# Optimization experiments

Measured on AMD Instinct MI355X. Metric: run time of the kernel, lower is better.

## Reference

```python
import jax, jax.numpy as jnp
import numpy as np

B_, L_, H_, N_ = 8, 1024, 1024, 64

def setup_inputs() -> dict:
    key = jax.random.key(0)
    k1, k2, k3, k4 = jax.random.split(key, 4)
    return {
        "samples": jax.random.normal(k1, (B_, L_, 3 * H_), dtype=jnp.float32),
        "label_one_hot": jax.random.uniform(k2, (B_, L_, N_), dtype=jnp.float32),
        "predict": jax.random.normal(k3, (B_, L_, N_), dtype=jnp.float32),
        "W": jax.random.normal(k4, (H_, 3 * H_), dtype=jnp.float32) * (1.0 / np.sqrt(3 * H_)),
        "b_proj": jnp.zeros((H_,), dtype=jnp.float32),
    }

def reference(samples, label_one_hot, predict, W, b_proj):
    # projection: Linear(3H -> H)
    s = jnp.einsum("blk,hk->blh", samples, W) + b_proj          # [b,L,H]
    # dense similarity graph with diagonal masked out, row-softmax
    graph = jnp.einsum("blh,bmh->blm", s, s)                     # [b,L,L]
    L = graph.shape[1]
    eye = jnp.eye(L, dtype=graph.dtype)
    A = jax.nn.softmax(graph - 1e5 * eye, axis=-1)               # [b,L,L]
    # centered masked labels
    sup = label_one_hot
    row_has = (jnp.sum(sup, axis=-1) > 0.5).astype(sup.dtype)    # [b,L]
    total = jnp.sum(row_has, axis=-1)[:, None]                   # [b,1]
    avg = (jnp.sum(sup, axis=-2) / total)[:, None, :]            # [b,1,N]
    B0 = (sup - avg) * row_has[..., None]                        # [b,L,N]
    # diagonal inverse-degree scaling (elementwise, no dense diag matmul)
    d = 1.0 / (jnp.sum(A, axis=-1) + 1e-10)                      # [b,L]
    P = d[:, :, None] * jnp.swapaxes(A, -1, -2)                  # [b,L,L]
    Db = d[:, :, None] * B0                                      # [b,L,N]
    # 6-step power-iteration scan with residual injection at t==3
    ut = jnp.zeros_like(B0)
    for t in range(1, 7):
        ut = jnp.einsum("blm,bmn->bln", P, ut) + Db
        if t == 3:
            ut = ut + predict  # dropout is identity in eval mode
    return ut

if __name__ == "__main__":
    out = reference(**setup_inputs())
    print(out.shape, out.dtype)
```

## Files before the change

kernel.cpp:

```cpp
#include <hip/hip_runtime.h>


typedef _Float16 f16_t;
typedef f16_t f16x4 __attribute__((ext_vector_type(4)));
typedef f16_t f16x8 __attribute__((ext_vector_type(8)));
typedef float floatx4 __attribute__((ext_vector_type(4)));

__device__ __forceinline__ void async_copy16(const void* g, void* l) {
  __builtin_amdgcn_global_load_lds(
      (const __attribute__((address_space(1))) void*)g,
      (__attribute__((address_space(3))) void*)l, 16, 0, 0);
}

__device__ __forceinline__ f16_t hi_of(float x) { return (f16_t)x; }
__device__ __forceinline__ f16_t lo_of(float x, f16_t h) {
  return (f16_t)(x - (float)h);
}

__global__ __launch_bounds__(256) void prep_kernel(
    const float* __restrict__ W, f16_t* __restrict__ Whi, f16_t* __restrict__ Wlo,
    const float* __restrict__ samples, f16_t* __restrict__ SampH)
{
  const int bx = blockIdx.x, tid = threadIdx.x;
  if (bx < 3072) {
    const int i = bx * 256 + tid;
    float4 v = ((const float4*)W)[i];
    v.x *= 32.f; v.y *= 32.f; v.z *= 32.f; v.w *= 32.f;
    f16x4 h, l;
    f16_t h0 = hi_of(v.x); h[0] = h0; l[0] = lo_of(v.x, h0);
    f16_t h1 = hi_of(v.y); h[1] = h1; l[1] = lo_of(v.y, h1);
    f16_t h2 = hi_of(v.z); h[2] = h2; l[2] = lo_of(v.z, h2);
    f16_t h3 = hi_of(v.w); h[3] = h3; l[3] = lo_of(v.w, h3);
    *(f16x4*)(Whi + (size_t)i * 4) = h;
    *(f16x4*)(Wlo + (size_t)i * 4) = l;
  } else {
    const int i = (bx - 3072) * 256 + tid;
    const float4 v = ((const float4*)samples)[i];
    f16x4 h;
    h[0] = (f16_t)v.x; h[1] = (f16_t)v.y; h[2] = (f16_t)v.z; h[3] = (f16_t)v.w;
    *(f16x4*)(SampH + (size_t)i * 4) = h;
  }
}

struct Frags {
  f16x8 a[8];
  f16x8 bh0, bh1, bl0, bl1;
};

#define DSR(dst_, addr_, OFFSTR_) \
  asm volatile("ds_read_b128 %0, %1 offset:" OFFSTR_ : "=v"(dst_) : "v"(addr_))

__device__ __forceinline__ void read_frags_asm(unsigned sa, unsigned sb,
                                               Frags& f) {
  DSR(f.bh0, sb, "0");
  DSR(f.bh1, sb, "1024");
  DSR(f.bl0, sb, "8192");
  DSR(f.bl1, sb, "9216");
  DSR(f.a[0], sa, "0");
  DSR(f.a[1], sa, "1024");
  DSR(f.a[2], sa, "2048");
  DSR(f.a[3], sa, "3072");
  DSR(f.a[4], sa, "4096");
  DSR(f.a[5], sa, "5120");
  DSR(f.a[6], sa, "6144");
  DSR(f.a[7], sa, "7168");
}

__global__ __launch_bounds__(512, 2) void gemm1_pipe(
    const f16_t* __restrict__ Ag,
    const f16_t* __restrict__ BhG, const f16_t* __restrict__ BlG,
    const float* __restrict__ bias,
    f16_t* __restrict__ Chi, f16_t* __restrict__ Clo,
    int N, int K, float cscale)
{
  __shared__ __align__(16) char smem[131072];

  const int tid = threadIdx.x;
  const int lane = tid & 63;
  const int wave = tid >> 6;
  const int wm = wave >> 2;
  const int wn = wave & 3;
  const int bid0 = blockIdx.y * 8 + blockIdx.x;
  const int xk = bid0 & 7, xj = bid0 >> 3;
  const int m0 = ((xk >> 1) * 8 + (xj >> 2)) * 256;
  const int n0 = ((xk & 1) * 4 + (xj & 3)) * 128;
  const int fr = lane & 15;
  const int lch = lane >> 4;

  const int gA0 = tid;
  const int gA1 = tid + 512;
  const int rA0 = gA0 >> 2, lcA0 = (gA0 & 3) ^ ((rA0 >> 1) & 3);
  const int rA1 = gA1 >> 2, lcA1 = (gA1 & 3) ^ ((rA1 >> 1) & 3);
  const int rB = tid >> 2, lcB = (tid & 3) ^ ((rB >> 1) & 3);
  const f16_t* aSrc0 = Ag + (size_t)(m0 + rA0) * K + lcA0 * 8;
  const f16_t* aSrc1 = Ag + (size_t)(m0 + rA1) * K + lcA1 * 8;
  const f16_t* bhSrc = BhG + (size_t)(n0 + rB) * K + lcB * 8;
  const f16_t* blSrc = BlG + (size_t)(n0 + rB) * K + lcB * 8;
  char* ldsA0 = smem + gA0 * 16;
  char* ldsA1 = smem + gA1 * 16;
  char* ldsBh = smem + 16384 + (size_t)tid * 16;
  char* ldsBl = smem + 24576 + (size_t)tid * 16;

  const int swz = (lch ^ ((fr >> 1) & 3)) * 16;
  const int aoff = (wm * 128 + fr) * 64 + swz;
  const int boff = (wn * 32 + fr) * 64 + swz;
  const unsigned ldsBase =
      (unsigned)(size_t)(__attribute__((address_space(3))) char*)smem;
  const unsigned aA0 = ldsBase + (unsigned)aoff;
  const unsigned aA1 = aA0 + 32768u;
  const unsigned aA2 = aA0 + 65536u;
  const unsigned aA3 = aA0 + 98304u;
  const unsigned bA0 = ldsBase + 16384u + (unsigned)boff;
  const unsigned bA1 = bA0 + 32768u;
  const unsigned bA2 = bA0 + 65536u;
  const unsigned bA3 = bA0 + 98304u;

  floatx4 acc[8][2] = {};
  const int NS = K >> 5;

#define STAGE(SS_, SLOT_)                                     \
  do {                                                        \
    int ss = (SS_); if (ss >= NS) ss -= NS;                   \
    const int k0 = ss * 32;                                   \
    async_copy16(aSrc0 + k0, ldsA0 + (SLOT_) * 32768);        \
    async_copy16(aSrc1 + k0, ldsA1 + (SLOT_) * 32768);        \
    async_copy16(bhSrc + k0, ldsBh + (SLOT_) * 32768);        \
    async_copy16(blSrc + k0, ldsBl + (SLOT_) * 32768);        \
  } while (0)

#define MFMA8(F_, P_)                                                                                               \
  do {                                                                                                              \
    acc[2*(P_)][0]   = __builtin_amdgcn_mfma_f32_16x16x32_f16((F_).a[2*(P_)],   (F_).bh0, acc[2*(P_)][0],   0,0,0); \
    acc[2*(P_)][1]   = __builtin_amdgcn_mfma_f32_16x16x32_f16((F_).a[2*(P_)],   (F_).bh1, acc[2*(P_)][1],   0,0,0); \
    acc[2*(P_)+1][0] = __builtin_amdgcn_mfma_f32_16x16x32_f16((F_).a[2*(P_)+1], (F_).bh0, acc[2*(P_)+1][0], 0,0,0); \
    acc[2*(P_)+1][1] = __builtin_amdgcn_mfma_f32_16x16x32_f16((F_).a[2*(P_)+1], (F_).bh1, acc[2*(P_)+1][1], 0,0,0); \
    acc[2*(P_)][0]   = __builtin_amdgcn_mfma_f32_16x16x32_f16((F_).a[2*(P_)],   (F_).bl0, acc[2*(P_)][0],   0,0,0); \
    acc[2*(P_)][1]   = __builtin_amdgcn_mfma_f32_16x16x32_f16((F_).a[2*(P_)],   (F_).bl1, acc[2*(P_)][1],   0,0,0); \
    acc[2*(P_)+1][0] = __builtin_amdgcn_mfma_f32_16x16x32_f16((F_).a[2*(P_)+1], (F_).bl0, acc[2*(P_)+1][0], 0,0,0); \
    acc[2*(P_)+1][1] = __builtin_amdgcn_mfma_f32_16x16x32_f16((F_).a[2*(P_)+1], (F_).bl1, acc[2*(P_)+1][1], 0,0,0); \
  } while (0)

#define SB0 __builtin_amdgcn_sched_barrier(0)

#define HALF(SPRE_, SLOTPRE_, ARD_, BRD_, FRD_, FMM_)            \
  do {                                                           \
    STAGE(SPRE_, SLOTPRE_);                                      \
    asm volatile("s_waitcnt vmcnt(8)" ::: "memory");             \
    __builtin_amdgcn_s_barrier();                                \
    DSR(FRD_.bh0, BRD_, "0");                                    \
    DSR(FRD_.bh1, BRD_, "1024");                                 \
    DSR(FRD_.bl0, BRD_, "8192");                                 \
    SB0;                                                         \
    asm volatile("s_waitcnt lgkmcnt(3)" ::: "memory");           \
    SB0;                                                         \
    __builtin_amdgcn_s_setprio(1);                               \
    MFMA8(FMM_, 0);                                              \
    __builtin_amdgcn_s_setprio(0);                               \
    SB0;                                                         \
    DSR(FRD_.bl1, BRD_, "9216");                                 \
    DSR(FRD_.a[0], ARD_, "0");                                   \
    DSR(FRD_.a[1], ARD_, "1024");                                \
    SB0;                                                         \
    __builtin_amdgcn_s_setprio(1);                               \
    MFMA8(FMM_, 1);                                              \
    __builtin_amdgcn_s_setprio(0);                               \
    SB0;                                                         \
    DSR(FRD_.a[2], ARD_, "2048");                                \
    DSR(FRD_.a[3], ARD_, "3072");                                \
    DSR(FRD_.a[4], ARD_, "4096");                                \
    SB0;                                                         \
    __builtin_amdgcn_s_setprio(1);                               \
    MFMA8(FMM_, 2);                                              \
    __builtin_amdgcn_s_setprio(0);                               \
    SB0;                                                         \
    DSR(FRD_.a[5], ARD_, "5120");                                \
    DSR(FRD_.a[6], ARD_, "6144");                                \
    DSR(FRD_.a[7], ARD_, "7168");                                \
    SB0;                                                         \
    __builtin_amdgcn_s_setprio(1);                               \
    MFMA8(FMM_, 3);                                              \
    __builtin_amdgcn_s_setprio(0);                               \
    SB0;                                                         \
  } while (0)

  Frags f0, f1;

  STAGE(0, 0); STAGE(1, 1); STAGE(2, 2);
  asm volatile("s_waitcnt vmcnt(8)" ::: "memory");
  __builtin_amdgcn_s_barrier();
  read_frags_asm(aA0, bA0, f0);
  SB0;

  for (int s = 0; s < NS; s += 4) {
    HALF(s + 3, 3, aA1, bA1, f1, f0);
    HALF(s + 4, 0, aA2, bA2, f0, f1);
    HALF(s + 5, 1, aA3, bA3, f1, f0);
    HALF(s + 6, 2, aA0, bA0, f0, f1);
  }
  asm volatile("s_waitcnt vmcnt(0)" ::: "memory");
#undef HALF
#undef STAGE
#undef MFMA8

  const int mr = (lane >> 4) * 4;
#pragma unroll
  for (int j = 0; j < 2; ++j) {
    const int n = n0 + wn * 32 + j * 16 + fr;
    const float bj = bias[n];
#pragma unroll
    for (int i = 0; i < 8; ++i) {
#pragma unroll
      for (int r = 0; r < 4; ++r) {
        const int m = m0 + wm * 128 + i * 16 + mr + r;
        float v = acc[i][j][r] * cscale + bj;
        f16_t h = hi_of(v);
        Chi[(size_t)m * N + n] = h;
        Clo[(size_t)m * N + n] = lo_of(v, h);
      }
    }
  }
}

struct Frags2 {
  f16x8 a[4];
  f16x8 bh[4];
  f16x8 bl[4];
};

__global__ __launch_bounds__(256, 2) void gemm2_pipe(
    const f16_t* __restrict__ Sh, const f16_t* __restrict__ Sl,
    float* __restrict__ Gf)
{
  const int K = 1024, N = 1024;
  const int batch = blockIdx.x & 7;
  const long long bo = (long long)batch * (1024LL * 1024);
  const f16_t* Ahi = Sh + bo;
  const f16_t* Bhi = Sh + bo;
  const f16_t* Blo = Sl + bo;
  float* Cf = Gf + bo;

  __shared__ __align__(16) char smem[73728];

  const int tid = threadIdx.x;
  const int lane = tid & 63;
  const int wave = tid >> 6;
  const int wm = wave >> 1, wn = wave & 1;

  int idx = blockIdx.x >> 3, ti = 0, accu = 0;
  while (accu + ti + 1 <= idx) { accu += ti + 1; ++ti; }
  const int m0 = ti * 128;
  const int n0 = (idx - accu) * 128;

  const int fr = lane & 15;
  const int lch = lane >> 4;

  const int gA0 = tid, gA1 = tid + 256;
  const int rA0 = gA0 >> 2, cA0 = (gA0 & 3) ^ ((rA0 >> 1) & 3);
  const int rA1 = gA1 >> 2, cA1 = (gA1 & 3) ^ ((rA1 >> 1) & 3);
  const f16_t* aSr0 = Ahi + (size_t)(m0 + rA0) * K + cA0 * 8;
  const f16_t* aSr1 = Ahi + (size_t)(m0 + rA1) * K + cA1 * 8;
  const f16_t* hSr0 = Bhi + (size_t)(n0 + rA0) * K + cA0 * 8;
  const f16_t* hSr1 = Bhi + (size_t)(n0 + rA1) * K + cA1 * 8;
  const f16_t* lSr0 = Blo + (size_t)(n0 + rA0) * K + cA0 * 8;
  const f16_t* lSr1 = Blo + (size_t)(n0 + rA1) * K + cA1 * 8;
  char* dA0 = smem + gA0 * 16;
  char* dA1 = smem + gA1 * 16;
  char* dH0 = smem + 8192 + gA0 * 16;
  char* dH1 = smem + 8192 + gA1 * 16;
  char* dL0 = smem + 16384 + gA0 * 16;
  char* dL1 = smem + 16384 + gA1 * 16;

  const int swz16 = (lch ^ ((fr >> 1) & 3)) * 16;
  const int aoff = (wm * 64 + fr) * 64 + swz16;
  const int boff = (wn * 64 + fr) * 64 + swz16;
  const unsigned ldsBase =
      (unsigned)(size_t)(__attribute__((address_space(3))) char*)smem;
  const unsigned aT0 = ldsBase + (unsigned)aoff;
  const unsigned aT1 = aT0 + 24576u;
  const unsigned aT2 = aT0 + 49152u;
  const unsigned bT0 = ldsBase + 8192u + (unsigned)boff;
  const unsigned bT1 = bT0 + 24576u;
  const unsigned bT2 = bT0 + 49152u;

  floatx4 acc[4][4] = {};
  const int NS = 32;

#define STAGE2(SS_, SLOT_)                                    \
  do {                                                        \
    int ss = (SS_); if (ss >= NS) ss -= NS;                   \
    const int k0 = ss * 32;                                   \
    async_copy16(aSr0 + k0, dA0 + (SLOT_) * 24576);           \
    async_copy16(aSr1 + k0, dA1 + (SLOT_) * 24576);           \
    async_copy16(hSr0 + k0, dH0 + (SLOT_) * 24576);           \
    async_copy16(hSr1 + k0, dH1 + (SLOT_) * 24576);           \
    async_copy16(lSr0 + k0, dL0 + (SLOT_) * 24576);           \
    async_copy16(lSr1 + k0, dL1 + (SLOT_) * 24576);           \
  } while (0)

#define MFMA8_2(F_, P_)                                                                              \
  do {                                                                                               \
    acc[0][P_] = __builtin_amdgcn_mfma_f32_16x16x32_f16((F_).a[0], (F_).bh[P_], acc[0][P_], 0,0,0);  \
    acc[1][P_] = __builtin_amdgcn_mfma_f32_16x16x32_f16((F_).a[1], (F_).bh[P_], acc[1][P_], 0,0,0);  \
    acc[2][P_] = __builtin_amdgcn_mfma_f32_16x16x32_f16((F_).a[2], (F_).bh[P_], acc[2][P_], 0,0,0);  \
    acc[3][P_] = __builtin_amdgcn_mfma_f32_16x16x32_f16((F_).a[3], (F_).bh[P_], acc[3][P_], 0,0,0);  \
    acc[0][P_] = __builtin_amdgcn_mfma_f32_16x16x32_f16((F_).a[0], (F_).bl[P_], acc[0][P_], 0,0,0);  \
    acc[1][P_] = __builtin_amdgcn_mfma_f32_16x16x32_f16((F_).a[1], (F_).bl[P_], acc[1][P_], 0,0,0);  \
    acc[2][P_] = __builtin_amdgcn_mfma_f32_16x16x32_f16((F_).a[2], (F_).bl[P_], acc[2][P_], 0,0,0);  \
    acc[3][P_] = __builtin_amdgcn_mfma_f32_16x16x32_f16((F_).a[3], (F_).bl[P_], acc[3][P_], 0,0,0);  \
  } while (0)

#define SB0 __builtin_amdgcn_sched_barrier(0)

#define GR3(SPRE_, SLOTPRE_, ARD_, BRD_, FRD_, FMM_)             \
  do {                                                           \
    STAGE2(SPRE_, SLOTPRE_);                                     \
    asm volatile("s_waitcnt vmcnt(6)" ::: "memory");             \
    __builtin_amdgcn_s_barrier();                                \
    DSR(FRD_.bh[0], BRD_, "0");                                  \
    DSR(FRD_.bh[1], BRD_, "1024");                               \
    DSR(FRD_.bh[2], BRD_, "2048");                               \
    SB0;                                                         \
    asm volatile("s_waitcnt lgkmcnt(3)" ::: "memory");           \
    SB0;                                                         \
    __builtin_amdgcn_s_setprio(1);                               \
    MFMA8_2(FMM_, 0);                                            \
    __builtin_amdgcn_s_setprio(0);                               \
    SB0;                                                         \
    DSR(FRD_.bh[3], BRD_, "3072");                               \
    DSR(FRD_.bl[0], BRD_, "8192");                               \
    DSR(FRD_.bl[1], BRD_, "9216");                               \
    SB0;                                                         \
    __builtin_amdgcn_s_setprio(1);                               \
    MFMA8_2(FMM_, 1);                                            \
    __builtin_amdgcn_s_setprio(0);                               \
    SB0;                                                         \
    DSR(FRD_.bl[2], BRD_, "10240");                              \
    DSR(FRD_.bl[3], BRD_, "11264");                              \
    DSR(FRD_.a[0], ARD_, "0");                                   \
    SB0;                                                         \
    __builtin_amdgcn_s_setprio(1);                               \
    MFMA8_2(FMM_, 2);                                            \
    __builtin_amdgcn_s_setprio(0);                               \
    SB0;                                                         \
    DSR(FRD_.a[1], ARD_, "1024");                                \
    DSR(FRD_.a[2], ARD_, "2048");                                \
    DSR(FRD_.a[3], ARD_, "3072");                                \
    SB0;                                                         \
    __builtin_amdgcn_s_setprio(1);                               \
    MFMA8_2(FMM_, 3);                                            \
    __builtin_amdgcn_s_setprio(0);                               \
    SB0;                                                         \
  } while (0)

  Frags2 f0, f1;

  STAGE2(0, 0); STAGE2(1, 1);
  asm volatile("s_waitcnt vmcnt(6)" ::: "memory");
  __builtin_amdgcn_s_barrier();
  DSR(f0.bh[0], bT0, "0");
  DSR(f0.bh[1], bT0, "1024");
  DSR(f0.bh[2], bT0, "2048");
  DSR(f0.bh[3], bT0, "3072");
  DSR(f0.bl[0], bT0, "8192");
  DSR(f0.bl[1], bT0, "9216");
  DSR(f0.bl[2], bT0, "10240");
  DSR(f0.bl[3], bT0, "11264");
  DSR(f0.a[0], aT0, "0");
  DSR(f0.a[1], aT0, "1024");
  DSR(f0.a[2], aT0, "2048");
  DSR(f0.a[3], aT0, "3072");
  SB0;

  for (int s = 0; s < 30; s += 6) {
    GR3(s + 2, 2, aT1, bT1, f1, f0);
    GR3(s + 3, 0, aT2, bT2, f0, f1);
    GR3(s + 4, 1, aT0, bT0, f1, f0);
    GR3(s + 5, 2, aT1, bT1, f0, f1);
    GR3(s + 6, 0, aT2, bT2, f1, f0);
    GR3(s + 7, 1, aT0, bT0, f0, f1);
  }
  asm volatile("s_waitcnt vmcnt(0)" ::: "memory");
  __builtin_amdgcn_s_barrier();
  DSR(f1.bh[0], bT1, "0");
  DSR(f1.bh[1], bT1, "1024");
  DSR(f1.bh[2], bT1, "2048");
  DSR(f1.bh[3], bT1, "3072");
  DSR(f1.bl[0], bT1, "8192");
  DSR(f1.bl[1], bT1, "9216");
  DSR(f1.bl[2], bT1, "10240");
  DSR(f1.bl[3], bT1, "11264");
  DSR(f1.a[0], aT1, "0");
  DSR(f1.a[1], aT1, "1024");
  DSR(f1.a[2], aT1, "2048");
  DSR(f1.a[3], aT1, "3072");
  SB0;
  asm volatile("s_waitcnt lgkmcnt(12)" ::: "memory");
  SB0;
  __builtin_amdgcn_s_setprio(1);
  MFMA8_2(f0, 0); MFMA8_2(f0, 1); MFMA8_2(f0, 2); MFMA8_2(f0, 3);
  __builtin_amdgcn_s_setprio(0);
  SB0;
  asm volatile("s_waitcnt lgkmcnt(0)" ::: "memory");
  SB0;
  __builtin_amdgcn_s_setprio(1);
  MFMA8_2(f1, 0); MFMA8_2(f1, 1); MFMA8_2(f1, 2); MFMA8_2(f1, 3);
  __builtin_amdgcn_s_setprio(0);
#undef GR3
#undef MFMA8_2
#undef STAGE2

  const int mr = (lane >> 4) * 4;
#pragma unroll
  for (int j = 0; j < 4; ++j) {
    const int n = n0 + wn * 64 + j * 16 + fr;
#pragma unroll
    for (int i = 0; i < 4; ++i) {
#pragma unroll
      for (int r = 0; r < 4; ++r) {
        const int m = m0 + wm * 64 + i * 16 + mr + r;
        float v = acc[i][j][r];
        if (m == n) v -= 1e5f;
        Cf[(size_t)m * N + n] = v;
      }
    }
  }

  if (m0 != n0) {
    float* T = (float*)smem;
#pragma unroll
    for (int mc = 0; mc < 4; ++mc) {
      __syncthreads();
      if (wm == (mc >> 1)) {
        const int ibase = (mc & 1) * 2;
#pragma unroll
        for (int di = 0; di < 2; ++di) {
#pragma unroll
          for (int j = 0; j < 4; ++j) {
            const int nl = wn * 64 + j * 16 + fr;
#pragma unroll
            for (int r = 0; r < 4; ++r) {
              const int mloc = di * 16 + mr + r;
              T[nl * 36 + mloc] = acc[ibase + di][j][r];
            }
          }
        }
      }
      __syncthreads();
      const int row = tid >> 1, half = tid & 1;
      const float* src = &T[row * 36 + half * 16];
      float* dst = Cf + (size_t)(n0 + row) * N + m0 + mc * 32 + half * 16;
#pragma unroll
      for (int q = 0; q < 16; ++q) dst[q] = src[q];
    }
  }
}

__global__ __launch_bounds__(256) void rowstats_kernel(
    const float* __restrict__ G, float* __restrict__ mx, float* __restrict__ inv)
{
  __shared__ float redm[4][4], reds[4][4], mxsh[4];
  const int tid = threadIdx.x;
  const int r0 = blockIdx.x * 4;
  const float* g = G + (size_t)r0 * 1024;
  const float4 v0 = ((const float4*)g)[tid];
  const float4 v1 = ((const float4*)(g + 1024))[tid];
  const float4 v2 = ((const float4*)(g + 2048))[tid];
  const float4 v3 = ((const float4*)(g + 3072))[tid];

  float m0 = fmaxf(fmaxf(v0.x, v0.y), fmaxf(v0.z, v0.w));
  float m1 = fmaxf(fmaxf(v1.x, v1.y), fmaxf(v1.z, v1.w));
  float m2 = fmaxf(fmaxf(v2.x, v2.y), fmaxf(v2.z, v2.w));
  float m3 = fmaxf(fmaxf(v3.x, v3.y), fmaxf(v3.z, v3.w));
#pragma unroll
  for (int off = 32; off > 0; off >>= 1) {
    m0 = fmaxf(m0, __shfl_down(m0, off));
    m1 = fmaxf(m1, __shfl_down(m1, off));
    m2 = fmaxf(m2, __shfl_down(m2, off));
    m3 = fmaxf(m3, __shfl_down(m3, off));
  }
  if ((tid & 63) == 0) {
    redm[0][tid >> 6] = m0; redm[1][tid >> 6] = m1;
    redm[2][tid >> 6] = m2; redm[3][tid >> 6] = m3;
  }
  __syncthreads();
  if (tid < 4)
    mxsh[tid] = fmaxf(fmaxf(redm[tid][0], redm[tid][1]),
                      fmaxf(redm[tid][2], redm[tid][3]));
  __syncthreads();
  const float M0 = mxsh[0], M1 = mxsh[1], M2 = mxsh[2], M3 = mxsh[3];

  float s0 = __expf(v0.x - M0) + __expf(v0.y - M0) + __expf(v0.z - M0) + __expf(v0.w - M0);
  float s1 = __expf(v1.x - M1) + __expf(v1.y - M1) + __expf(v1.z - M1) + __expf(v1.w - M1);
  float s2 = __expf(v2.x - M2) + __expf(v2.y - M2) + __expf(v2.z - M2) + __expf(v2.w - M2);
  float s3 = __expf(v3.x - M3) + __expf(v3.y - M3) + __expf(v3.z - M3) + __expf(v3.w - M3);
#pragma unroll
  for (int off = 32; off > 0; off >>= 1) {
    s0 += __shfl_down(s0, off);
    s1 += __shfl_down(s1, off);
    s2 += __shfl_down(s2, off);
    s3 += __shfl_down(s3, off);
  }
  if ((tid & 63) == 0) {
    reds[0][tid >> 6] = s0; reds[1][tid >> 6] = s1;
    reds[2][tid >> 6] = s2; reds[3][tid >> 6] = s3;
  }
  __syncthreads();
  if (tid < 4) {
    mx[r0 + tid] = mxsh[tid];
    inv[r0 + tid] = 1.0f /
        (reds[tid][0] + reds[tid][1] + reds[tid][2] + reds[tid][3]);
  }
}

__global__ __launch_bounds__(256) void make_at_kernel(
    const float* __restrict__ G, const float* __restrict__ mx,
    const float* __restrict__ inv, f16_t* __restrict__ At)
{
  const int r0 = blockIdx.x * 4;
  const int b = r0 >> 10;
  const int tid = threadIdx.x;
  const float4 m = ((const float4*)(mx + b * 1024))[tid];
  const float4 iv = ((const float4*)(inv + b * 1024))[tid];
#pragma unroll
  for (int k = 0; k < 4; ++k) {
    const float4 g = ((const float4*)(G + (size_t)(r0 + k) * 1024))[tid];
    f16x4 o;
    o[0] = (f16_t)(__expf(g.x - m.x) * iv.x);
    o[1] = (f16_t)(__expf(g.y - m.y) * iv.y);
    o[2] = (f16_t)(__expf(g.z - m.z) * iv.z);
    o[3] = (f16_t)(__expf(g.w - m.w) * iv.w);
    *(f16x4*)(At + (size_t)(r0 + k) * 1024 + tid * 4) = o;
  }
}

__global__ __launch_bounds__(256) void db_stats(
    const float* __restrict__ sup, float* __restrict__ colpart,
    float* __restrict__ totalpart)
{
  const int b = blockIdx.x >> 4, chunk = blockIdx.x & 15;
  const int tid = threadIdx.x;
  const int r = tid >> 2, q = tid & 3;
  const float* s = sup + ((size_t)b * 1024 + chunk * 64 + r) * 64 + q * 16;
  const float4 x0 = ((const float4*)s)[0];
  const float4 x1 = ((const float4*)s)[1];
  const float4 x2 = ((const float4*)s)[2];
  const float4 x3 = ((const float4*)s)[3];

  float rs = (x0.x + x0.y + x0.z + x0.w) + (x1.x + x1.y + x1.z + x1.w) +
             (x2.x + x2.y + x2.z + x2.w) + (x3.x + x3.y + x3.z + x3.w);
  rs += __shfl_xor(rs, 1);
  rs += __shfl_xor(rs, 2);
  const float rh = (rs > 0.5f) ? 1.f : 0.f;

  __shared__ float colp[64];
  __shared__ float tp[4];
  if (tid < 64) colp[tid] = 0.f;
  __syncthreads();
  atomicAdd(&colp[q * 16 + 0], x0.x);  atomicAdd(&colp[q * 16 + 1], x0.y);
  atomicAdd(&colp[q * 16 + 2], x0.z);  atomicAdd(&colp[q * 16 + 3], x0.w);
  atomicAdd(&colp[q * 16 + 4], x1.x);  atomicAdd(&colp[q * 16 + 5], x1.y);
  atomicAdd(&colp[q * 16 + 6], x1.z);  atomicAdd(&colp[q * 16 + 7], x1.w);
  atomicAdd(&colp[q * 16 + 8], x2.x);  atomicAdd(&colp[q * 16 + 9], x2.y);
  atomicAdd(&colp[q * 16 + 10], x2.z); atomicAdd(&colp[q * 16 + 11], x2.w);
  atomicAdd(&colp[q * 16 + 12], x3.x); atomicAdd(&colp[q * 16 + 13], x3.y);
  atomicAdd(&colp[q * 16 + 14], x3.z); atomicAdd(&colp[q * 16 + 15], x3.w);

  float ts = (q == 0) ? rh : 0.f;
#pragma unroll
  for (int off = 32; off > 0; off >>= 1) ts += __shfl_down(ts, off);
  if ((tid & 63) == 0) tp[tid >> 6] = ts;
  __syncthreads();
  if (tid < 64) colpart[((size_t)b * 16 + chunk) * 64 + tid] = colp[tid];
  if (tid == 0) totalpart[b * 16 + chunk] = tp[0] + tp[1] + tp[2] + tp[3];
}

__global__ __launch_bounds__(256) void db_apply(
    const float* __restrict__ sup, const float* __restrict__ colpart,
    const float* __restrict__ totalpart,
    float* __restrict__ Db, f16_t* __restrict__ DbT)
{
  const int b = blockIdx.x >> 4, chunk = blockIdx.x & 15;
  const int tid = threadIdx.x;
  const int r = tid >> 2, q = tid & 3;

  __shared__ float avgsh[64];
  __shared__ float totsh;
  __shared__ f16_t DbTs[64 * 72];

  float a = 0.f;
  if (tid < 64) {
#pragma unroll
    for (int c = 0; c < 16; ++c) a += colpart[((size_t)b * 16 + c) * 64 + tid];
  }
  if (tid == 0) {
    float tt = 0.f;
#pragma unroll
    for (int c = 0; c < 16; ++c) tt += totalpart[b * 16 + c];
    totsh = tt;
  }
  __syncthreads();
  if (tid < 64) avgsh[tid] = a / totsh;
  __syncthreads();

  const size_t rowoff = ((size_t)b * 1024 + chunk * 64 + r) * 64 + q * 16;
  const float* s = sup + rowoff;
  float4 x0 = ((const float4*)s)[0];
  float4 x1 = ((const float4*)s)[1];
  float4 x2 = ((const float4*)s)[2];
  float4 x3 = ((const float4*)s)[3];

  float rs = (x0.x + x0.y + x0.z + x0.w) + (x1.x + x1.y + x1.z + x1.w) +
             (x2.x + x2.y + x2.z + x2.w) + (x3.x + x3.y + x3.z + x3.w);
  rs += __shfl_xor(rs, 1);
  rs += __shfl_xor(rs, 2);
  const float rh = (rs > 0.5f) ? 1.f : 0.f;

  const int nb = q * 16;
  x0.x = (x0.x - avgsh[nb + 0]) * rh;  x0.y = (x0.y - avgsh[nb + 1]) * rh;
  x0.z = (x0.z - avgsh[nb + 2]) * rh;  x0.w = (x0.w - avgsh[nb + 3]) * rh;
  x1.x = (x1.x - avgsh[nb + 4]) * rh;  x1.y = (x1.y - avgsh[nb + 5]) * rh;
  x1.z = (x1.z - avgsh[nb + 6]) * rh;  x1.w = (x1.w - avgsh[nb + 7]) * rh;
  x2.x = (x2.x - avgsh[nb + 8]) * rh;  x2.y = (x2.y - avgsh[nb + 9]) * rh;
  x2.z = (x2.z - avgsh[nb + 10]) * rh; x2.w = (x2.w - avgsh[nb + 11]) * rh;
  x3.x = (x3.x - avgsh[nb + 12]) * rh; x3.y = (x3.y - avgsh[nb + 13]) * rh;
  x3.z = (x3.z - avgsh[nb + 14]) * rh; x3.w = (x3.w - avgsh[nb + 15]) * rh;

  float* d = Db + rowoff;
  ((float4*)d)[0] = x0; ((float4*)d)[1] = x1;
  ((float4*)d)[2] = x2; ((float4*)d)[3] = x3;

  DbTs[(nb + 0) * 72 + r] = (f16_t)x0.x;  DbTs[(nb + 1) * 72 + r] = (f16_t)x0.y;
  DbTs[(nb + 2) * 72 + r] = (f16_t)x0.z;  DbTs[(nb + 3) * 72 + r] = (f16_t)x0.w;
  DbTs[(nb + 4) * 72 + r] = (f16_t)x1.x;  DbTs[(nb + 5) * 72 + r] = (f16_t)x1.y;
  DbTs[(nb + 6) * 72 + r] = (f16_t)x1.z;  DbTs[(nb + 7) * 72 + r] = (f16_t)x1.w;
  DbTs[(nb + 8) * 72 + r] = (f16_t)x2.x;  DbTs[(nb + 9) * 72 + r] = (f16_t)x2.y;
  DbTs[(nb + 10) * 72 + r] = (f16_t)x2.z; DbTs[(nb + 11) * 72 + r] = (f16_t)x2.w;
  DbTs[(nb + 12) * 72 + r] = (f16_t)x3.x; DbTs[(nb + 13) * 72 + r] = (f16_t)x3.y;
  DbTs[(nb + 14) * 72 + r] = (f16_t)x3.z; DbTs[(nb + 15) * 72 + r] = (f16_t)x3.w;
  __syncthreads();

  const int n = tid >> 2, seg = tid & 3;
  const f16_t* src = &DbTs[n * 72 + seg * 16];
  f16_t* dst = DbT + ((size_t)b * 64 + n) * 1024 + chunk * 64 + seg * 16;
  *(f16x8*)dst = *(const f16x8*)src;
  *(f16x8*)(dst + 8) = *(const f16x8*)(src + 8);
}

template <int PRED, int FINAL>
__global__ __launch_bounds__(256) void iter_step(
    const f16_t* __restrict__ At, const f16_t* __restrict__ UT,
    const float* __restrict__ Db, const float* __restrict__ Pred,
    f16_t* __restrict__ UTn, float* __restrict__ OutF)
{
  const int L = 1024, Nn = 64;
  const int b = blockIdx.x & 7, l0 = (blockIdx.x >> 3) * 32;
  At += (size_t)b * L * L;
  UT += (size_t)b * Nn * L;

  __shared__ __align__(16) char smem[131072];

  const int tid = threadIdx.x;
  const int lane = tid & 63;
  const int wave = tid >> 6;
  const int fr = lane & 15;
  const int lch = lane >> 4;
  const int mwb = wave * 256;

  int g_, rw_, sc_;
  g_ = lane;        rw_ = g_ >> 3; sc_ = (g_ & 7) ^ (rw_ & 7);
  const f16_t* aS0 = At + (size_t)(l0 + rw_) * L + mwb + sc_ * 8;
  g_ = lane + 64;   rw_ = g_ >> 3; sc_ = (g_ & 7) ^ (rw_ & 7);
  const f16_t* aS1 = At + (size_t)(l0 + rw_) * L + mwb + sc_ * 8;
  g_ = lane + 128;  rw_ = g_ >> 3; sc_ = (g_ & 7) ^ (rw_ & 7);
  const f16_t* aS2 = At + (size_t)(l0 + rw_) * L + mwb + sc_ * 8;
  g_ = lane + 192;  rw_ = g_ >> 3; sc_ = (g_ & 7) ^ (rw_ & 7);
  const f16_t* aS3 = At + (size_t)(l0 + rw_) * L + mwb + sc_ * 8;
  g_ = lane;        rw_ = g_ >> 3; sc_ = (g_ & 7) ^ (rw_ & 7);
  const f16_t* uS0 = UT + (size_t)rw_ * L + mwb + sc_ * 8;
  g_ = lane + 64;   rw_ = g_ >> 3; sc_ = (g_ & 7) ^ (rw_ & 7);
  const f16_t* uS1 = UT + (size_t)rw_ * L + mwb + sc_ * 8;
  g_ = lane + 128;  rw_ = g_ >> 3; sc_ = (g_ & 7) ^ (rw_ & 7);
  const f16_t* uS2 = UT + (size_t)rw_ * L + mwb + sc_ * 8;
  g_ = lane + 192;  rw_ = g_ >> 3; sc_ = (g_ & 7) ^ (rw_ & 7);
  const f16_t* uS3 = UT + (size_t)rw_ * L + mwb + sc_ * 8;
  g_ = lane + 256;  rw_ = g_ >> 3; sc_ = (g_ & 7) ^ (rw_ & 7);
  const f16_t* uS4 = UT + (size_t)rw_ * L + mwb + sc_ * 8;
  g_ = lane + 320;  rw_ = g_ >> 3; sc_ = (g_ & 7) ^ (rw_ & 7);
  const f16_t* uS5 = UT + (size_t)rw_ * L + mwb + sc_ * 8;
  g_ = lane + 384;  rw_ = g_ >> 3; sc_ = (g_ & 7) ^ (rw_ & 7);
  const f16_t* uS6 = UT + (size_t)rw_ * L + mwb + sc_ * 8;
  g_ = lane + 448;  rw_ = g_ >> 3; sc_ = (g_ & 7) ^ (rw_ & 7);
  const f16_t* uS7 = UT + (size_t)rw_ * L + mwb + sc_ * 8;

  char* stA = smem + wave * 24576;
  char* stU = stA + 4096;

  const int offK0 = fr * 128 + ((lch ^ (fr & 7)) * 16);
  const int offK1 = fr * 128 + (((4 + lch) ^ (fr & 7)) * 16);

  floatx4 acc[2][4] = {};

#define STG(M0_, BUF_)                                        \
  do {                                                        \
    char* dA = stA + (BUF_) * 12288;                          \
    char* dU = stU + (BUF_) * 12288;                          \
    async_copy16(aS0 + (M0_), dA + lane * 16);                \
    async_copy16(aS1 + (M0_), dA + 1024 + lane * 16);         \
    async_copy16(aS2 + (M0_), dA + 2048 + lane * 16);         \
    async_copy16(aS3 + (M0_), dA + 3072 + lane * 16);         \
    async_copy16(uS0 + (M0_), dU + lane * 16);                \
    async_copy16(uS1 + (M0_), dU + 1024 + lane * 16);         \
    async_copy16(uS2 + (M0_), dU + 2048 + lane * 16);         \
    async_copy16(uS3 + (M0_), dU + 3072 + lane * 16);         \
    async_copy16(uS4 + (M0_), dU + 4096 + lane * 16);         \
    async_copy16(uS5 + (M0_), dU + 5120 + lane * 16);         \
    async_copy16(uS6 + (M0_), dU + 6144 + lane * 16);         \
    async_copy16(uS7 + (M0_), dU + 7168 + lane * 16);         \
  } while (0)

#define LD8(b_, o_) (*(const f16x8*)((b_) + (o_)))
#define MM(A_, U_, C_) C_ = __builtin_amdgcn_mfma_f32_16x16x32_f16(A_, U_, C_, 0, 0, 0)

#define CHUNK(BUF_)                                                       \
  do {                                                                    \
    const char* cA = stA + (BUF_) * 12288;                                \
    const char* cU = stU + (BUF_) * 12288;                                \
    f16x8 a00 = LD8(cA, offK0), a01 = LD8(cA, offK1);                     \
    f16x8 a10 = LD8(cA, offK0 + 2048), a11 = LD8(cA, offK1 + 2048);       \
    f16x8 u00 = LD8(cU, offK0), u01 = LD8(cU, offK1);                     \
    f16x8 u10 = LD8(cU, offK0 + 2048), u11 = LD8(cU, offK1 + 2048);       \
    f16x8 u20 = LD8(cU, offK0 + 4096), u21 = LD8(cU, offK1 + 4096);       \
    f16x8 u30 = LD8(cU, offK0 + 6144), u31 = LD8(cU, offK1 + 6144);       \
    MM(a00, u00, acc[0][0]); MM(a00, u10, acc[0][1]);                     \
    MM(a00, u20, acc[0][2]); MM(a00, u30, acc[0][3]);                     \
    MM(a10, u00, acc[1][0]); MM(a10, u10, acc[1][1]);                     \
    MM(a10, u20, acc[1][2]); MM(a10, u30, acc[1][3]);                     \
    MM(a01, u01, acc[0][0]); MM(a01, u11, acc[0][1]);                     \
    MM(a01, u21, acc[0][2]); MM(a01, u31, acc[0][3]);                     \
    MM(a11, u01, acc[1][0]); MM(a11, u11, acc[1][1]);                     \
    MM(a11, u21, acc[1][2]); MM(a11, u31, acc[1][3]);                     \
  } while (0)

#define SB0 __builtin_amdgcn_sched_barrier(0)

  STG(0, 0);
  STG(64, 1);
  asm volatile("s_waitcnt vmcnt(12)" ::: "memory");
  SB0;
  CHUNK(0);
  SB0;
  STG(128, 0);
  asm volatile("s_waitcnt vmcnt(12)" ::: "memory");
  SB0;
  CHUNK(1);
  SB0;
  STG(192, 1);
  asm volatile("s_waitcnt vmcnt(12)" ::: "memory");
  SB0;
  CHUNK(0);
  SB0;
  asm volatile("s_waitcnt vmcnt(0)" ::: "memory");
  SB0;
  CHUNK(1);
#undef CHUNK
#undef STG

  float* P = (float*)(smem + 98304) + wave * 2048;
  const int mr = (lane >> 4) * 4;
#pragma unroll
  for (int li = 0; li < 2; ++li)
#pragma unroll
    for (int j = 0; j < 4; ++j)
#pragma unroll
      for (int r = 0; r < 4; ++r)
        P[(li * 16 + mr + r) * 64 + j * 16 + fr] = acc[li][j][r];
  __syncthreads();

  const float* P0 = (const float*)(smem + 98304);
  const size_t obase = ((size_t)b * L + l0) * Nn;
  f16_t* OutS = (f16_t*)smem;
#pragma unroll
  for (int it = 0; it < 2; ++it) {
    const int e4 = it * 256 + tid;
    const int l = e4 >> 4, n4 = (e4 & 15) * 4;
    const int eo = l * 64 + n4;
    float4 v = *(const float4*)(P0 + eo);
    const float4 p1 = *(const float4*)(P0 + 2048 + eo);
    const float4 p2 = *(const float4*)(P0 + 4096 + eo);
    const float4 p3 = *(const float4*)(P0 + 6144 + eo);
    v.x += p1.x; v.y += p1.y; v.z += p1.z; v.w += p1.w;
    v.x += p2.x; v.y += p2.y; v.z += p2.z; v.w += p2.w;
    v.x += p3.x; v.y += p3.y; v.z += p3.z; v.w += p3.w;
    const float4 d = *(const float4*)(Db + obase + eo);
    v.x += d.x; v.y += d.y; v.z += d.z; v.w += d.w;
    if (PRED) {
      const float4 p = *(const float4*)(Pred + obase + eo);
      v.x += p.x; v.y += p.y; v.z += p.z; v.w += p.w;
    }
    if (FINAL) {
      *(float4*)(OutF + obase + eo) = v;
    } else {
      OutS[(n4 + 0) * 40 + l] = (f16_t)v.x;
      OutS[(n4 + 1) * 40 + l] = (f16_t)v.y;
      OutS[(n4 + 2) * 40 + l] = (f16_t)v.z;
      OutS[(n4 + 3) * 40 + l] = (f16_t)v.w;
    }
  }
  if (!FINAL) {
    __syncthreads();
    f16_t* dst = UTn + (size_t)b * Nn * L + l0;
    const int n = tid >> 2, lc = (tid & 3) * 8;
    *(f16x8*)(dst + (size_t)n * L + lc) = *(const f16x8*)&OutS[n * 40 + lc];
  }
#undef SB0
#undef LD8
#undef MM
}

extern "C" void kernel_launch(void* const* d_in, const int* in_sizes, int n_in,
                              void* d_out, int out_size, void* d_ws, size_t ws_size,
                              hipStream_t stream) {
  const float* samples = (const float*)d_in[0];
  const float* label   = (const float*)d_in[1];
  const float* predict = (const float*)d_in[2];
  const float* W       = (const float*)d_in[3];
  const float* bproj   = (const float*)d_in[4];
  float* out = (float*)d_out;

  char* ws = (char*)d_ws;
  f16_t* Whi = (f16_t*)ws;
  f16_t* Wlo = (f16_t*)(ws + 6291456);
  float* mx  = (float*)ws;
  float* inv = (float*)(ws + 32768);
  float* Db  = (float*)(ws + 65536);
  f16_t* DbT = (f16_t*)(ws + 65536 + 2097152);
  f16_t* UTa = (f16_t*)(ws + 65536 + 3145728);
  f16_t* UTb = (f16_t*)(ws + 65536 + 4194304);
  float* colpart   = (float*)(ws + 5308416);
  float* totalpart = (float*)(ws + 5308416 + 32768);
  f16_t* SampH = (f16_t*)(ws + 12582912);
  float* G     = (float*)(ws + 12582912);
  f16_t* Shi = (f16_t*)(ws + 62914560);
  f16_t* Slo = (f16_t*)(ws + 62914560 + 16777216);
  f16_t* At  = Shi;

  prep_kernel<<<dim3(27648), 256, 0, stream>>>(W, Whi, Wlo, samples, SampH);

  gemm1_pipe<<<dim3(8, 32), 512, 0, stream>>>(
      SampH, Whi, Wlo, bproj, Shi, Slo, 1024, 3072, 1.0f / 32.0f);

  gemm2_pipe<<<dim3(288), 256, 0, stream>>>(Shi, Slo, G);

  rowstats_kernel<<<2048, 256, 0, stream>>>(G, mx, inv);
  make_at_kernel<<<2048, 256, 0, stream>>>(G, mx, inv, At);

  db_stats<<<128, 256, 0, stream>>>(label, colpart, totalpart);
  db_apply<<<128, 256, 0, stream>>>(label, colpart, totalpart, Db, DbT);

  iter_step<0, 0><<<dim3(256), 256, 0, stream>>>(At, DbT, Db, nullptr, UTa, nullptr);
  iter_step<1, 0><<<dim3(256), 256, 0, stream>>>(At, UTa, Db, predict, UTb, nullptr);
  iter_step<0, 0><<<dim3(256), 256, 0, stream>>>(At, UTb, Db, nullptr, UTa, nullptr);
  iter_step<0, 0><<<dim3(256), 256, 0, stream>>>(At, UTa, Db, nullptr, UTb, nullptr);
  iter_step<0, 1><<<dim3(256), 256, 0, stream>>>(At, UTb, Db, nullptr, nullptr, out);
}
```

Before: 339.2 us.

## Load B fragments directly from global into registers, bypassing LDS

The projection GEMM now stages only the A tile through LDS. Each wave loads its B (W hi/lo) fragments straight from global memory into registers with global_load_dwordx4, issued one stage ahead. This halves LDS usage to 64KB and removes the LDS writes and reads for B. In exchange, B reuse across the waves sharing the same wn is lost, so global/L2 traffic goes up, and the vmcnt accounting becomes more fragile.

```diff
diff --git a/kernel.cpp b/kernel.cpp
--- a/kernel.cpp
+++ b/kernel.cpp
@@ -50,21 +50,8 @@
 #define DSR(dst_, addr_, OFFSTR_) \
   asm volatile("ds_read_b128 %0, %1 offset:" OFFSTR_ : "=v"(dst_) : "v"(addr_))
 
-__device__ __forceinline__ void read_frags_asm(unsigned sa, unsigned sb,
-                                               Frags& f) {
-  DSR(f.bh0, sb, "0");
-  DSR(f.bh1, sb, "1024");
-  DSR(f.bl0, sb, "8192");
-  DSR(f.bl1, sb, "9216");
-  DSR(f.a[0], sa, "0");
-  DSR(f.a[1], sa, "1024");
-  DSR(f.a[2], sa, "2048");
-  DSR(f.a[3], sa, "3072");
-  DSR(f.a[4], sa, "4096");
-  DSR(f.a[5], sa, "5120");
-  DSR(f.a[6], sa, "6144");
-  DSR(f.a[7], sa, "7168");
-}
+#define GLD(dst_, ptr_) \
+  asm volatile("global_load_dwordx4 %0, %1, off" : "=v"(dst_) : "v"(ptr_))
 
 __global__ __launch_bounds__(512, 2) void gemm1_pipe(
     const f16_t* __restrict__ Ag,
@@ -73,7 +60,7 @@
     f16_t* __restrict__ Chi, f16_t* __restrict__ Clo,
     int N, int K, float cscale)
 {
-  __shared__ __align__(16) char smem[131072];
+  __shared__ __align__(16) char smem[65536];
 
   const int tid = threadIdx.x;
   const int lane = tid & 63;
@@ -91,41 +78,44 @@
   const int gA1 = tid + 512;
   const int rA0 = gA0 >> 2, lcA0 = (gA0 & 3) ^ ((rA0 >> 1) & 3);
   const int rA1 = gA1 >> 2, lcA1 = (gA1 & 3) ^ ((rA1 >> 1) & 3);
-  const int rB = tid >> 2, lcB = (tid & 3) ^ ((rB >> 1) & 3);
   const f16_t* aSrc0 = Ag + (size_t)(m0 + rA0) * K + lcA0 * 8;
   const f16_t* aSrc1 = Ag + (size_t)(m0 + rA1) * K + lcA1 * 8;
-  const f16_t* bhSrc = BhG + (size_t)(n0 + rB) * K + lcB * 8;
-  const f16_t* blSrc = BlG + (size_t)(n0 + rB) * K + lcB * 8;
   char* ldsA0 = smem + gA0 * 16;
   char* ldsA1 = smem + gA1 * 16;
-  char* ldsBh = smem + 16384 + (size_t)tid * 16;
-  char* ldsBl = smem + 24576 + (size_t)tid * 16;
+
+  const f16_t* bh0Src = BhG + (size_t)(n0 + wn * 32 + fr) * K + lch * 8;
+  const f16_t* bh1Src = BhG + (size_t)(n0 + wn * 32 + 16 + fr) * K + lch * 8;
+  const f16_t* bl0Src = BlG + (size_t)(n0 + wn * 32 + fr) * K + lch * 8;
+  const f16_t* bl1Src = BlG + (size_t)(n0 + wn * 32 + 16 + fr) * K + lch * 8;
 
   const int swz = (lch ^ ((fr >> 1) & 3)) * 16;
   const int aoff = (wm * 128 + fr) * 64 + swz;
-  const int boff = (wn * 32 + fr) * 64 + swz;
   const unsigned ldsBase =
       (unsigned)(size_t)(__attribute__((address_space(3))) char*)smem;
   const unsigned aA0 = ldsBase + (unsigned)aoff;
-  const unsigned aA1 = aA0 + 32768u;
-  const unsigned aA2 = aA0 + 65536u;
-  const unsigned aA3 = aA0 + 98304u;
-  const unsigned bA0 = ldsBase + 16384u + (unsigned)boff;
-  const unsigned bA1 = bA0 + 32768u;
-  const unsigned bA2 = bA0 + 65536u;
-  const unsigned bA3 = bA0 + 98304u;
+  const unsigned aA1 = aA0 + 16384u;
+  const unsigned aA2 = aA0 + 32768u;
+  const unsigned aA3 = aA0 + 49152u;
 
   floatx4 acc[8][2] = {};
   const int NS = K >> 5;
 
-#define STAGE(SS_, SLOT_)                                     \
+#define STAGEA(SS_, SLOT_)                                    \
   do {                                                        \
     int ss = (SS_); if (ss >= NS) ss -= NS;                   \
     const int k0 = ss * 32;                                   \
-    async_copy16(aSrc0 + k0, ldsA0 + (SLOT_) * 32768);        \
-    async_copy16(aSrc1 + k0, ldsA1 + (SLOT_) * 32768);        \
-    async_copy16(bhSrc + k0, ldsBh + (SLOT_) * 32768);        \
-    async_copy16(blSrc + k0, ldsBl + (SLOT_) * 32768);        \
+    async_copy16(aSrc0 + k0, ldsA0 + (SLOT_) * 16384);        \
+    async_copy16(aSrc1 + k0, ldsA1 + (SLOT_) * 16384);        \
+  } while (0)
+
+#define LOADB(SS_, FRD_)                                      \
+  do {                                                        \
+    int sb = (SS_); if (sb >= NS) sb -= NS;                   \
+    const int kb = sb * 32;                                   \
+    GLD(FRD_.bh0, bh0Src + kb);                               \
+    GLD(FRD_.bh1, bh1Src + kb);                               \
+    GLD(FRD_.bl0, bl0Src + kb);                               \
+    GLD(FRD_.bl1, bl1Src + kb);                               \
   } while (0)
 
 #define MFMA8(F_, P_)                                                                                               \
@@ -142,38 +132,35 @@
 
 #define SB0 __builtin_amdgcn_sched_barrier(0)
 
-#define HALF(SPRE_, SLOTPRE_, ARD_, BRD_, FRD_, FMM_)            \
+#define HALF(SPRE_, SLOTPRE_, ARD_, FRD_, FMM_)                  \
   do {                                                           \
-    STAGE(SPRE_, SLOTPRE_);                                      \
-    asm volatile("s_waitcnt vmcnt(8)" ::: "memory");             \
+    LOADB((SPRE_) - 2, FRD_);                                    \
+    STAGEA(SPRE_, SLOTPRE_);                                     \
+    asm volatile("s_waitcnt vmcnt(12)" ::: "memory");            \
     __builtin_amdgcn_s_barrier();                                \
-    DSR(FRD_.bh0, BRD_, "0");                                    \
-    DSR(FRD_.bh1, BRD_, "1024");                                 \
-    DSR(FRD_.bl0, BRD_, "8192");                                 \
-    SB0;                                                         \
-    asm volatile("s_waitcnt lgkmcnt(3)" ::: "memory");           \
+    DSR(FRD_.a[0], ARD_, "0");                                   \
+    DSR(FRD_.a[1], ARD_, "1024");                                \
+    SB0;                                                         \
+    asm volatile("s_waitcnt lgkmcnt(2) vmcnt(8)" ::: "memory");  \
     SB0;                                                         \
     __builtin_amdgcn_s_setprio(1);                               \
     MFMA8(FMM_, 0);                                              \
     __builtin_amdgcn_s_setprio(0);                               \
     SB0;                                                         \
-    DSR(FRD_.bl1, BRD_, "9216");                                 \
-    DSR(FRD_.a[0], ARD_, "0");                                   \
-    DSR(FRD_.a[1], ARD_, "1024");                                \
+    DSR(FRD_.a[2], ARD_, "2048");                                \
+    DSR(FRD_.a[3], ARD_, "3072");                                \
     SB0;                                                         \
     __builtin_amdgcn_s_setprio(1);                               \
     MFMA8(FMM_, 1);                                              \
     __builtin_amdgcn_s_setprio(0);                               \
     SB0;                                                         \
-    DSR(FRD_.a[2], ARD_, "2048");                                \
-    DSR(FRD_.a[3], ARD_, "3072");                                \
     DSR(FRD_.a[4], ARD_, "4096");                                \
+    DSR(FRD_.a[5], ARD_, "5120");                                \
     SB0;                                                         \
     __builtin_amdgcn_s_setprio(1);                               \
     MFMA8(FMM_, 2);                                              \
     __builtin_amdgcn_s_setprio(0);                               \
     SB0;                                                         \
-    DSR(FRD_.a[5], ARD_, "5120");                                \
     DSR(FRD_.a[6], ARD_, "6144");                                \
     DSR(FRD_.a[7], ARD_, "7168");                                \
     SB0;                                                         \
@@ -185,21 +172,32 @@
 
   Frags f0, f1;
 
-  STAGE(0, 0); STAGE(1, 1); STAGE(2, 2);
+  STAGEA(0, 0);
+  STAGEA(1, 1);
+  LOADB(0, f0);
+  STAGEA(2, 2);
   asm volatile("s_waitcnt vmcnt(8)" ::: "memory");
   __builtin_amdgcn_s_barrier();
-  read_frags_asm(aA0, bA0, f0);
+  DSR(f0.a[0], aA0, "0");
+  DSR(f0.a[1], aA0, "1024");
+  DSR(f0.a[2], aA0, "2048");
+  DSR(f0.a[3], aA0, "3072");
+  DSR(f0.a[4], aA0, "4096");
+  DSR(f0.a[5], aA0, "5120");
+  DSR(f0.a[6], aA0, "6144");
+  DSR(f0.a[7], aA0, "7168");
   SB0;
 
   for (int s = 0; s < NS; s += 4) {
-    HALF(s + 3, 3, aA1, bA1, f1, f0);
-    HALF(s + 4, 0, aA2, bA2, f0, f1);
-    HALF(s + 5, 1, aA3, bA3, f1, f0);
-    HALF(s + 6, 2, aA0, bA0, f0, f1);
+    HALF(s + 3, 3, aA1, f1, f0);
+    HALF(s + 4, 0, aA2, f0, f1);
+    HALF(s + 5, 1, aA3, f1, f0);
+    HALF(s + 6, 2, aA0, f0, f1);
   }
   asm volatile("s_waitcnt vmcnt(0)" ::: "memory");
 #undef HALF
-#undef STAGE
+#undef STAGEA
+#undef LOADB
 #undef MFMA8
 
   const int mr = (lane >> 4) * 4;
```

Measured after the change: 369.4 us. +8.9%, slower.
